# Optimization experiments

Measured on AMD Instinct MI355X. Metric: run time of the kernel, lower is better.

## Reference

```python
import jax, jax.numpy as jnp
import numpy as np

NUM_HEADS = 16
D_MODEL = 1024
HEAD_DIM = D_MODEL // NUM_HEADS
SCALE = float(np.sqrt(HEAD_DIM))  # NOTE: original multiplies q by sqrt(head_dim)
EPS = 1e-5


def layernorm(x, g, b):
    # LayerNorm over last dim (head_dim), learnable affine
    mu = jnp.mean(x, axis=-1, keepdims=True)
    var = jnp.mean(jnp.square(x - mu), axis=-1, keepdims=True)
    return (x - mu) * jax.lax.rsqrt(var + EPS) * g + b


def setup_inputs() -> dict:
    key = jax.random.key(0)
    ks = jax.random.split(key, 8)
    B, Nq, Nc = 2, 2048, 2048
    s = 0.02
    return {
        "x_query": jax.random.normal(ks[0], (B, Nq, D_MODEL), jnp.float32),
        "x_context": jax.random.normal(ks[1], (B, Nc, D_MODEL), jnp.float32),
        "Wq": jax.random.normal(ks[2], (D_MODEL, D_MODEL), jnp.float32) * s,
        "Wkv": jax.random.normal(ks[3], (D_MODEL, 2 * D_MODEL), jnp.float32) * s,
        "Wp": jax.random.normal(ks[4], (D_MODEL, D_MODEL), jnp.float32) * s,
        "bp": jnp.zeros((D_MODEL,), jnp.float32),
        "ln_g": jnp.ones((HEAD_DIM,), jnp.float32),
        "ln_b": jnp.zeros((HEAD_DIM,), jnp.float32),
    }


def reference(x_query, x_context, Wq, Wkv, Wp, bp, ln_g, ln_b):
    B, Nq, _ = x_query.shape
    Nc = x_context.shape[1]
    H, D = NUM_HEADS, HEAD_DIM
    # projections
    q = (x_query @ Wq).reshape(B, Nq, H, D).transpose(0, 2, 1, 3)  # b h n d
    kv = (x_context @ Wkv).reshape(B, Nc, 2, H, D)
    k = kv[:, :, 0].transpose(0, 2, 1, 3)  # b h n d
    v = kv[:, :, 1].transpose(0, 2, 1, 3)
    # QK-LayerNorm (shared params)
    q = layernorm(q, ln_g, ln_b)
    k = layernorm(k, ln_g, ln_b)
    # NOTE: faithful to source — q is MULTIPLIED by sqrt(head_dim)
    q = q * SCALE
    attn = jnp.einsum("bhqd,bhkd->bhqk", q, k)
    attn = jax.nn.softmax(attn, axis=-1)
    out = jnp.einsum("bhqk,bhkd->bhqd", attn, v)
    out = out.transpose(0, 2, 1, 3).reshape(B, Nq, H * D)
    return out @ Wp + bp
```

## Files before the change

### kernel.cpp

```cpp
#include <hip/hip_runtime.h>
#include <stdint.h>

#define NUM_HEADS 16
#define HEAD_DIM 64
#define D_MODEL 1024
#define SEQ 2048
#define BATCH 2

typedef unsigned short u16;
typedef _Float16 f16x8 __attribute__((ext_vector_type(8)));
typedef float f32x4 __attribute__((ext_vector_type(4)));

__device__ __forceinline__ u16 f2h(float f) {
    _Float16 h = (_Float16)f;
    return __builtin_bit_cast(u16, h);
}
__device__ __forceinline__ float h2f(u16 h) {
    return (float)__builtin_bit_cast(_Float16, h);
}
__device__ __forceinline__ uint32_t pkrtz(float a, float b) {
    return __builtin_bit_cast(uint32_t, __builtin_amdgcn_cvt_pkrtz(a, b));
}
__device__ __forceinline__ uint32_t pkrtn(float a, float b) {
    return (uint32_t)f2h(a) | ((uint32_t)f2h(b) << 16);
}

__device__ __forceinline__ float ex2(float x) {
#if __has_builtin(__builtin_amdgcn_exp2f)
    return __builtin_amdgcn_exp2f(x);
#else
    float r;
    asm("v_exp_f32 %0, %1" : "=v"(r) : "v"(x));
    return r;
#endif
}

__device__ __forceinline__ f16x8 ld8h(const u16* p) {
    return *reinterpret_cast<const f16x8*>(p);
}

__device__ __forceinline__ void gl_lds16(const void* g, void* l) {
    __builtin_amdgcn_global_load_lds(
        (const __attribute__((address_space(1))) void*)g,
        (__attribute__((address_space(3))) void*)l,
        16, 0, 0);
}

template <int CTRL>
__device__ __forceinline__ float dpp_mov(float x) {
    return __builtin_bit_cast(float,
        __builtin_amdgcn_update_dpp(0, __builtin_bit_cast(int, x), CTRL, 0xf, 0xf, true));
}
__device__ __forceinline__ float rowsum16(float x) {
    x += dpp_mov<0x121>(x);
    x += dpp_mov<0x122>(x);
    x += dpp_mov<0x124>(x);
    x += dpp_mov<0x128>(x);
    return x;
}

__global__ __launch_bounds__(256) void k_prep(const float* __restrict__ xq,
                                              const float* __restrict__ xc,
                                              const float* __restrict__ Wq,
                                              const float* __restrict__ Wkv,
                                              const float* __restrict__ Wp,
                                              u16* __restrict__ xq16,
                                              u16* __restrict__ xc16,
                                              u16* __restrict__ WqT16,
                                              u16* __restrict__ WkvT16,
                                              u16* __restrict__ WpT16) {
    __shared__ float tile[32][33];
    const int t = blockIdx.x;
    if (t < 8192) {
        int i = t * 256 + threadIdx.x;
        const float* src; u16* dst; int j;
        if (i < 1048576) { src = xq; dst = xq16; j = i; }
        else             { src = xc; dst = xc16; j = i - 1048576; }
        float4 v = reinterpret_cast<const float4*>(src)[j];
        ushort4 o;
        o.x = f2h(v.x); o.y = f2h(v.y); o.z = f2h(v.z); o.w = f2h(v.w);
        reinterpret_cast<ushort4*>(dst)[j] = o;
        return;
    }
    const float* W; u16* WT; int N, bi;
    if (t < 9216)       { W = Wq;  WT = WqT16;  N = 1024; bi = t - 8192; }
    else if (t < 11264) { W = Wkv; WT = WkvT16; N = 2048; bi = t - 9216; }
    else                { W = Wp;  WT = WpT16;  N = 1024; bi = t - 11264; }
    const int K = 1024;
    const int nb = N / 32;
    const int bn = (bi % nb) * 32, bk = (bi / nb) * 32;
    const int tx = threadIdx.x & 31;
    const int ty = threadIdx.x >> 5;
#pragma unroll
    for (int i = 0; i < 32; i += 8)
        tile[ty + i][tx] = W[(size_t)(bk + ty + i) * N + bn + tx];
    __syncthreads();
#pragma unroll
    for (int i = 0; i < 32; i += 8)
        WT[(size_t)(bn + ty + i) * K + bk + tx] = f2h(tile[tx][ty + i]);
}

__device__ __forceinline__ void gemm_mainloop_f16(const u16* __restrict__ A,
                                                  const u16* __restrict__ Bt,
                                                  u16* As, u16* Bs,
                                                  int tileM, int tileN, int K,
                                                  f32x4 acc[4][4]) {
    const int tid = threadIdx.x;
    const int lane = tid & 63;
    const int wv = tid >> 6;
    const int wm = wv >> 1, wn = wv & 1;
    const int quad = lane >> 4, l15 = lane & 15;

    const int c0 = tid, c1 = tid + 256;
    const u16* Ap0 = A + (size_t)(tileM + (c0 >> 2)) * K + (c0 & 3) * 8;
    const u16* Ap1 = A + (size_t)(tileM + (c1 >> 2)) * K + (c1 & 3) * 8;
    const u16* Bp0 = Bt + (size_t)(tileN + (c0 >> 2)) * K + (c0 & 3) * 8;
    const u16* Bp1 = Bt + (size_t)(tileN + (c1 >> 2)) * K + (c1 & 3) * 8;

    gl_lds16(Ap0, &As[c0 * 8]);
    gl_lds16(Ap1, &As[c1 * 8]);
    gl_lds16(Bp0, &Bs[c0 * 8]);
    gl_lds16(Bp1, &Bs[c1 * 8]);

    for (int k0 = 0; k0 < K; k0 += 32) {
        __syncthreads();
        const int cb = (k0 >> 5) & 1;
        if (k0 + 32 < K) {
            const int nbuf = cb ^ 1;
            gl_lds16(Ap0 + k0 + 32, &As[nbuf * 4096 + c0 * 8]);
            gl_lds16(Ap1 + k0 + 32, &As[nbuf * 4096 + c1 * 8]);
            gl_lds16(Bp0 + k0 + 32, &Bs[nbuf * 4096 + c0 * 8]);
            gl_lds16(Bp1 + k0 + 32, &Bs[nbuf * 4096 + c1 * 8]);
        }
        const int cbo = cb * 4096;
        f16x8 af[4], bfr[4];
#pragma unroll
        for (int mi = 0; mi < 4; ++mi)
            af[mi] = ld8h(&As[cbo + (wm * 64 + mi * 16 + l15) * 32 + quad * 8]);
#pragma unroll
        for (int ni = 0; ni < 4; ++ni)
            bfr[ni] = ld8h(&Bs[cbo + (wn * 64 + ni * 16 + l15) * 32 + quad * 8]);
#pragma unroll
        for (int mi = 0; mi < 4; ++mi)
#pragma unroll
            for (int ni = 0; ni < 4; ++ni)
                acc[mi][ni] = __builtin_amdgcn_mfma_f32_16x16x32_f16(
                    af[mi], bfr[ni], acc[mi][ni], 0, 0, 0);
    }
}

#define ACC_INIT()                                                   \
    f32x4 acc[4][4];                                                 \
    _Pragma("unroll") for (int i = 0; i < 4; ++i)                    \
        _Pragma("unroll") for (int j = 0; j < 4; ++j)                \
            acc[i][j] = (f32x4){0.f, 0.f, 0.f, 0.f};

__global__ __launch_bounds__(256, 2) void k_proj_f16(const u16* __restrict__ xq16,
                                                     const u16* __restrict__ xc16,
                                                     const u16* __restrict__ WqT16,
                                                     const u16* __restrict__ WkvT16,
                                                     const float* __restrict__ lng,
                                                     const float* __restrict__ lnb,
                                                     u16* __restrict__ Qh_h,
                                                     u16* __restrict__ Qh_l,
                                                     u16* __restrict__ Kh,
                                                     u16* __restrict__ VT) {
    __shared__ __align__(16) u16 As[2 * 128 * 32];
    __shared__ __align__(16) u16 Bs[2 * 128 * 32];
    const int bx = blockIdx.x;
    const int tileM = blockIdx.y * 128;
    const int tid = threadIdx.x;
    const int lane = tid & 63;
    const int wv = tid >> 6;
    const int wm = wv >> 1, wn = wv & 1;
    const int quad = lane >> 4, l15 = lane & 15;
    ACC_INIT();

    if (bx < 16) {
        const bool isQ = bx < 8;
        const int tileN = (bx & 7) * 128;
        const u16* Axx = isQ ? xq16 : xc16;
        const u16* Bt  = isQ ? WqT16 : WkvT16;
        const float scl = isQ ? 11.5415603294809528f : 1.0f;

        gemm_mainloop_f16(Axx, Bt, As, Bs, tileM, tileN, D_MODEL, acc);

        float gv[4], bv[4];
#pragma unroll
        for (int ni = 0; ni < 4; ++ni) { gv[ni] = lng[ni * 16 + l15]; bv[ni] = lnb[ni * 16 + l15]; }

#pragma unroll
        for (int mi = 0; mi < 4; ++mi) {
#pragma unroll
            for (int r = 0; r < 4; ++r) {
                float sum = 0.f, sq = 0.f;
#pragma unroll
                for (int ni = 0; ni < 4; ++ni) { float x = acc[mi][ni][r]; sum += x; sq += x * x; }
                sum = rowsum16(sum);
                sq  = rowsum16(sq);
                float mu = sum * (1.f / 64.f);
                float var = sq * (1.f / 64.f) - mu * mu;
                float rs = rsqrtf(var + 1e-5f);
                int m = tileM + wm * 64 + mi * 16 + quad * 4 + r;
                int bb = m >> 11, n = m & (SEQ - 1);
#pragma unroll
                for (int ni = 0; ni < 4; ++ni) {
                    int colg = tileN + wn * 64 + ni * 16 + l15;
                    int h = colg >> 6;
                    float y = ((acc[mi][ni][r] - mu) * rs * gv[ni] + bv[ni]) * scl;
                    size_t idx = (((size_t)bb * NUM_HEADS + h) * SEQ + n) * HEAD_DIM + (colg & 63);
                    u16 yh = f2h(y);
                    if (isQ) {
                        Qh_h[idx] = yh;
                        Qh_l[idx] = f2h(y - h2f(yh));
                    } else {
                        Kh[idx] = yh;
                    }
                }
            }
        }
    } else {
        const int tileN = D_MODEL + (bx - 16) * 128;
        gemm_mainloop_f16(xc16, WkvT16, As, Bs, tileM, tileN, D_MODEL, acc);
#pragma unroll
        for (int mi = 0; mi < 4; ++mi) {
            int m0 = tileM + wm * 64 + mi * 16 + quad * 4;
            int bb = m0 >> 11, n0 = m0 & (SEQ - 1);
#pragma unroll
            for (int ni = 0; ni < 4; ++ni) {
                int colg = tileN + wn * 64 + ni * 16 + l15 - D_MODEL;
                int h = colg >> 6, d = colg & 63;
                ushort4 o;
                o.x = f2h(acc[mi][ni][0]);
                o.y = f2h(acc[mi][ni][1]);
                o.z = f2h(acc[mi][ni][2]);
                o.w = f2h(acc[mi][ni][3]);
                *reinterpret_cast<ushort4*>(
                    &VT[(((size_t)bb * NUM_HEADS + h) * HEAD_DIM + d) * SEQ + n0]) = o;
            }
        }
    }
}

__global__ __launch_bounds__(256, 2) void k_gemm_out(const u16* __restrict__ A,
                                                     const u16* __restrict__ Bt,
                                                     const float* __restrict__ bp,
                                                     float* __restrict__ out) {
    __shared__ __align__(16) u16 As[2 * 128 * 32];
    __shared__ __align__(16) u16 Bs[2 * 128 * 32];
    const int tileM = blockIdx.y * 128, tileN = blockIdx.x * 128;
    const int tid = threadIdx.x;
    const int lane = tid & 63;
    const int wv = tid >> 6;
    const int wm = wv >> 1, wn = wv & 1;
    const int quad = lane >> 4, l15 = lane & 15;
    ACC_INIT();
    gemm_mainloop_f16(A, Bt, As, Bs, tileM, tileN, D_MODEL, acc);

    float bpv[4];
#pragma unroll
    for (int ni = 0; ni < 4; ++ni) bpv[ni] = bp[tileN + wn * 64 + ni * 16 + l15];
#pragma unroll
    for (int mi = 0; mi < 4; ++mi) {
#pragma unroll
        for (int r = 0; r < 4; ++r) {
            int m = tileM + wm * 64 + mi * 16 + quad * 4 + r;
#pragma unroll
            for (int ni = 0; ni < 4; ++ni) {
                int colg = tileN + wn * 64 + ni * 16 + l15;
                out[(size_t)m * D_MODEL + colg] = acc[mi][ni][r] + bpv[ni];
            }
        }
    }
}

__global__ __launch_bounds__(256) void k_attn(const u16* __restrict__ Qh_h,
                                              const u16* __restrict__ Qh_l,
                                              const u16* __restrict__ Kh,
                                              const u16* __restrict__ VT,
                                              u16* __restrict__ AO) {
    __shared__ __align__(16) u16 Ks[2 * 64 * 64];
    __shared__ __align__(16) u16 Vs[2 * 64 * 64];
    __shared__ __align__(16) u16 Ps[64 * 64];

    const int tid = threadIdx.x;
    const int lane = tid & 63;
    const int wv = tid >> 6;
    const int quad = lane >> 4, l15 = lane & 15;
    const int sw = l15 & 3;
    const int w1 = (l15 >> 2) & 1;
    const int id = blockIdx.x;
    const int bh = (id & 7) | (((id >> 8) & 3) << 3);
    const int qt = (id >> 3) & 31;

    const size_t bh_off = (size_t)bh * SEQ * HEAD_DIM;
    const u16* Vbh = VT + (size_t)bh * HEAD_DIM * SEQ;

    f16x8 qfh[2], qfl[2];
#pragma unroll
    for (int kt = 0; kt < 2; ++kt) {
        size_t off = bh_off + (size_t)(qt * 64 + wv * 16 + l15) * HEAD_DIM + kt * 32 + quad * 8;
        qfh[kt] = ld8h(Qh_h + off);
        qfl[kt] = ld8h(Qh_l + off);
    }

    f16x8 ones;
#pragma unroll
    for (int i = 0; i < 8; ++i) ones[i] = (_Float16)1.0f;

    const int rr = lane >> 3;
    const int ss = lane & 7;
    const int cc = ss ^ rr;
    const int row0 = wv * 16 + rr;
    const u16* k0 = Kh + bh_off + (size_t)row0 * HEAD_DIM + cc * 8;
    const u16* v0 = Vbh + (size_t)row0 * SEQ + cc * 8;
    const int ldsW = (wv * 16) * 64;

    f32x4 acc_o[4];
    f32x4 acc_l = (f32x4){0.f, 0.f, 0.f, 0.f};
    float m_i = -3.0e38f;
#pragma unroll
    for (int ni = 0; ni < 4; ++ni) acc_o[ni] = (f32x4){0.f, 0.f, 0.f, 0.f};

    gl_lds16(k0,                &Ks[ldsW]);
    gl_lds16(k0 + 8 * HEAD_DIM, &Ks[ldsW + 8 * 64]);
    gl_lds16(v0,                &Vs[ldsW]);
    gl_lds16(v0 + 8 * SEQ,      &Vs[ldsW + 8 * 64]);

    const int psRow = (wv * 16 + l15) * 64;
    const int psW = psRow + (quad ^ (w1 << 1)) * 4;

    for (int j = 0; j < SEQ / 64; ++j) {
        __syncthreads();
        if (j + 1 < SEQ / 64) {
            const int nb = (j + 1) & 1;
            const size_t ko = (size_t)(j + 1) * 64 * HEAD_DIM;
            const int vo = (j + 1) * 64;
            gl_lds16(k0 + ko,                &Ks[nb * 4096 + ldsW]);
            gl_lds16(k0 + ko + 8 * HEAD_DIM, &Ks[nb * 4096 + ldsW + 8 * 64]);
            gl_lds16(v0 + vo,                &Vs[nb * 4096 + ldsW]);
            gl_lds16(v0 + vo + 8 * SEQ,      &Vs[nb * 4096 + ldsW + 8 * 64]);
        }
        const int bb = (j & 1) * 4096;

        f32x4 acc_s[4];
#pragma unroll
        for (int ni = 0; ni < 4; ++ni) acc_s[ni] = (f32x4){0.f, 0.f, 0.f, 0.f};
#pragma unroll
        for (int kt = 0; kt < 2; ++kt) {
            f16x8 kf[4];
#pragma unroll
            for (int ni = 0; ni < 4; ++ni) {
                int slot = (kt * 4 + quad) ^ (l15 & 7);
                kf[ni] = ld8h(&Ks[bb + (ni * 16 + l15) * 64 + slot * 8]);
            }
#pragma unroll
            for (int ni = 0; ni < 4; ++ni) {
                acc_s[ni] = __builtin_amdgcn_mfma_f32_16x16x32_f16(
                    kf[ni], qfh[kt], acc_s[ni], 0, 0, 0);
                acc_s[ni] = __builtin_amdgcn_mfma_f32_16x16x32_f16(
                    kf[ni], qfl[kt], acc_s[ni], 0, 0, 0);
            }
        }

        float mn[4];
#pragma unroll
        for (int ni = 0; ni < 4; ++ni)
            mn[ni] = fmaxf(fmaxf(acc_s[ni][0], acc_s[ni][1]),
                           fmaxf(acc_s[ni][2], acc_s[ni][3]));
        float mx = fmaxf(fmaxf(mn[0], mn[1]), fmaxf(mn[2], mn[3]));
        mx = fmaxf(mx, __shfl_xor(mx, 16, 64));
        mx = fmaxf(mx, __shfl_xor(mx, 32, 64));
        float mnew = fmaxf(m_i, mx);
        if (__any(mx > m_i)) {
            float alpha = ex2(m_i - mnew);
#pragma unroll
            for (int ni = 0; ni < 4; ++ni) acc_o[ni] *= alpha;
            acc_l[0] *= alpha;
            m_i = mnew;
        }
#pragma unroll
        for (int ni = 0; ni < 4; ++ni) {
            float p0 = ex2(acc_s[ni][0] - mnew);
            float p1 = ex2(acc_s[ni][1] - mnew);
            float p2 = ex2(acc_s[ni][2] - mnew);
            float p3 = ex2(acc_s[ni][3] - mnew);
            uint2 u;
            u.x = pkrtz(p0, p1);
            u.y = pkrtz(p2, p3);
            *reinterpret_cast<uint2*>(&Ps[psW + ((ni ^ sw) * 16)]) = u;
        }

#pragma unroll
        for (int kt = 0; kt < 2; ++kt) {
            int pchunk = (kt * 2 + (quad >> 1)) ^ sw;
            f16x8 pf = ld8h(&Ps[psRow + pchunk * 16 + (((quad & 1) ^ w1) * 8)]);
            f16x8 vf[4];
#pragma unroll
            for (int ni = 0; ni < 4; ++ni) {
                int slot = (kt * 4 + quad) ^ (l15 & 7);
                vf[ni] = ld8h(&Vs[bb + (ni * 16 + l15) * 64 + slot * 8]);
            }
#pragma unroll
            for (int ni = 0; ni < 4; ++ni)
                acc_o[ni] = __builtin_amdgcn_mfma_f32_16x16x32_f16(
                    vf[ni], pf, acc_o[ni], 0, 0, 0);
            acc_l = __builtin_amdgcn_mfma_f32_16x16x32_f16(
                ones, pf, acc_l, 0, 0, 0);
        }
    }

    const float inv = 1.0f / acc_l[0];
#pragma unroll
    for (int ni = 0; ni < 4; ++ni) {
        uint2 u;
        u.x = pkrtn(acc_o[ni][0] * inv, acc_o[ni][1] * inv);
        u.y = pkrtn(acc_o[ni][2] * inv, acc_o[ni][3] * inv);
        *reinterpret_cast<uint2*>(&Ps[psW + ((ni ^ sw) * 16)]) = u;
    }
    const int b = bh >> 4, h = bh & 15;
    const int qrow = qt * 64 + wv * 16 + l15;
    const int echunk = quad ^ sw;
    uint4 o0 = *reinterpret_cast<const uint4*>(&Ps[psRow + echunk * 16 + w1 * 8]);
    uint4 o1 = *reinterpret_cast<const uint4*>(&Ps[psRow + echunk * 16 + (1 - w1) * 8]);
    size_t outb = ((size_t)(b * SEQ + qrow)) * D_MODEL + h * 64 + quad * 16;
    *reinterpret_cast<uint4*>(&AO[outb])     = o0;
    *reinterpret_cast<uint4*>(&AO[outb + 8]) = o1;
}

extern "C" void kernel_launch(void* const* d_in, const int* in_sizes, int n_in,
                              void* d_out, int out_size, void* d_ws, size_t ws_size,
                              hipStream_t stream) {
    const float* xq  = (const float*)d_in[0];
    const float* xc  = (const float*)d_in[1];
    const float* Wq  = (const float*)d_in[2];
    const float* Wkv = (const float*)d_in[3];
    const float* Wp  = (const float*)d_in[4];
    const float* bp  = (const float*)d_in[5];
    const float* lng = (const float*)d_in[6];
    const float* lnb = (const float*)d_in[7];
    float* out = (float*)d_out;

    char* ws = (char*)d_ws;
    const size_t MB = 1 << 20;
    u16* xq16   = (u16*)(ws + 0 * MB);
    u16* xc16   = (u16*)(ws + 8 * MB);
    u16* WqT16  = (u16*)(ws + 16 * MB);
    u16* WkvT16 = (u16*)(ws + 18 * MB);
    u16* WpT16  = (u16*)(ws + 22 * MB);
    u16* Qh_h   = (u16*)(ws + 24 * MB);
    u16* Qh_l   = (u16*)(ws + 32 * MB);
    u16* Kh     = (u16*)(ws + 40 * MB);
    u16* VT     = (u16*)(ws + 48 * MB);
    u16* AO     = xq16;

    k_prep<<<12288, 256, 0, stream>>>(xq, xc, Wq, Wkv, Wp,
                                      xq16, xc16, WqT16, WkvT16, WpT16);
    k_proj_f16<<<dim3(24, 32), 256, 0, stream>>>(xq16, xc16, WqT16, WkvT16,
                                                 lng, lnb, Qh_h, Qh_l, Kh, VT);
    k_attn<<<1024, 256, 0, stream>>>(Qh_h, Qh_l, Kh, VT, AO);
    k_gemm_out<<<dim3(8, 32), 256, 0, stream>>>(AO, WpT16, bp, out);
}
```

Before: 241.4 us.

## Remap GEMM blocks per XCD, shrink output GEMM tile, raise attention MFMA priority

The projection and output GEMMs now use a flat 1D grid that maps consecutive M tiles onto the same XCD, so blocks sharing rows of A hit the same L2. The output GEMM moves to 128x64 tiles with its own mainloop, doubling the block count to 512 so the GPU's compute units fill better. The attention kernel wraps its two MFMA phases in s_setprio(1) to favour matrix issue over other waves. The smaller output tile lowers per-block reuse, and the priority hints may or may not help scheduling.

```diff
diff --git a/kernel.cpp b/kernel.cpp
--- a/kernel.cpp
+++ b/kernel.cpp
@@ -167,8 +167,11 @@
                                                      u16* __restrict__ VT) {
     __shared__ __align__(16) u16 As[2 * 128 * 32];
     __shared__ __align__(16) u16 Bs[2 * 128 * 32];
-    const int bx = blockIdx.x;
-    const int tileM = blockIdx.y * 128;
+    const int flat = blockIdx.x;
+    const int xcd = flat & 7;
+    const int j = flat >> 3;
+    const int bx = j >> 2;
+    const int tileM = (xcd * 4 + (j & 3)) * 128;
     const int tid = threadIdx.x;
     const int lane = tid & 63;
     const int wv = tid >> 6;
@@ -247,27 +250,70 @@
                                                      const float* __restrict__ bp,
                                                      float* __restrict__ out) {
     __shared__ __align__(16) u16 As[2 * 128 * 32];
-    __shared__ __align__(16) u16 Bs[2 * 128 * 32];
-    const int tileM = blockIdx.y * 128, tileN = blockIdx.x * 128;
+    __shared__ __align__(16) u16 Bs[2 * 64 * 32];
+    const int flat = blockIdx.x;
+    const int xcd = flat & 7;
+    const int j = flat >> 3;
+    const int tileM = (xcd * 4 + (j & 3)) * 128;
+    const int tileN = (j >> 2) * 64;
     const int tid = threadIdx.x;
     const int lane = tid & 63;
     const int wv = tid >> 6;
     const int wm = wv >> 1, wn = wv & 1;
     const int quad = lane >> 4, l15 = lane & 15;
-    ACC_INIT();
-    gemm_mainloop_f16(A, Bt, As, Bs, tileM, tileN, D_MODEL, acc);
-
-    float bpv[4];
-#pragma unroll
-    for (int ni = 0; ni < 4; ++ni) bpv[ni] = bp[tileN + wn * 64 + ni * 16 + l15];
+    const int K = D_MODEL;
+
+    f32x4 acc[4][2];
+#pragma unroll
+    for (int i = 0; i < 4; ++i)
+#pragma unroll
+        for (int n = 0; n < 2; ++n) acc[i][n] = (f32x4){0.f, 0.f, 0.f, 0.f};
+
+    const int c0 = tid, c1 = tid + 256;
+    const u16* Ap0 = A + (size_t)(tileM + (c0 >> 2)) * K + (c0 & 3) * 8;
+    const u16* Ap1 = A + (size_t)(tileM + (c1 >> 2)) * K + (c1 & 3) * 8;
+    const u16* Bp0 = Bt + (size_t)(tileN + (c0 >> 2)) * K + (c0 & 3) * 8;
+
+    gl_lds16(Ap0, &As[c0 * 8]);
+    gl_lds16(Ap1, &As[c1 * 8]);
+    gl_lds16(Bp0, &Bs[c0 * 8]);
+
+    for (int k0 = 0; k0 < K; k0 += 32) {
+        __syncthreads();
+        const int cb = (k0 >> 5) & 1;
+        if (k0 + 32 < K) {
+            const int nbuf = cb ^ 1;
+            gl_lds16(Ap0 + k0 + 32, &As[nbuf * 4096 + c0 * 8]);
+            gl_lds16(Ap1 + k0 + 32, &As[nbuf * 4096 + c1 * 8]);
+            gl_lds16(Bp0 + k0 + 32, &Bs[nbuf * 2048 + c0 * 8]);
+        }
+        const int ao = cb * 4096, bo = cb * 2048;
+        f16x8 af[4], bfr[2];
+#pragma unroll
+        for (int mi = 0; mi < 4; ++mi)
+            af[mi] = ld8h(&As[ao + (wm * 64 + mi * 16 + l15) * 32 + quad * 8]);
+#pragma unroll
+        for (int ni = 0; ni < 2; ++ni)
+            bfr[ni] = ld8h(&Bs[bo + (wn * 32 + ni * 16 + l15) * 32 + quad * 8]);
+#pragma unroll
+        for (int mi = 0; mi < 4; ++mi)
+#pragma unroll
+            for (int ni = 0; ni < 2; ++ni)
+                acc[mi][ni] = __builtin_amdgcn_mfma_f32_16x16x32_f16(
+                    af[mi], bfr[ni], acc[mi][ni], 0, 0, 0);
+    }
+
+    float bpv[2];
+#pragma unroll
+    for (int ni = 0; ni < 2; ++ni) bpv[ni] = bp[tileN + wn * 32 + ni * 16 + l15];
 #pragma unroll
     for (int mi = 0; mi < 4; ++mi) {
 #pragma unroll
         for (int r = 0; r < 4; ++r) {
             int m = tileM + wm * 64 + mi * 16 + quad * 4 + r;
 #pragma unroll
-            for (int ni = 0; ni < 4; ++ni) {
-                int colg = tileN + wn * 64 + ni * 16 + l15;
+            for (int ni = 0; ni < 2; ++ni) {
+                int colg = tileN + wn * 32 + ni * 16 + l15;
                 out[(size_t)m * D_MODEL + colg] = acc[mi][ni][r] + bpv[ni];
             }
         }
@@ -346,6 +392,7 @@
         f32x4 acc_s[4];
 #pragma unroll
         for (int ni = 0; ni < 4; ++ni) acc_s[ni] = (f32x4){0.f, 0.f, 0.f, 0.f};
+        __builtin_amdgcn_s_setprio(1);
 #pragma unroll
         for (int kt = 0; kt < 2; ++kt) {
             f16x8 kf[4];
@@ -362,6 +409,7 @@
                     kf[ni], qfl[kt], acc_s[ni], 0, 0, 0);
             }
         }
+        __builtin_amdgcn_s_setprio(0);
 
         float mn[4];
 #pragma unroll
@@ -391,6 +439,7 @@
             *reinterpret_cast<uint2*>(&Ps[psW + ((ni ^ sw) * 16)]) = u;
         }
 
+        __builtin_amdgcn_s_setprio(1);
 #pragma unroll
         for (int kt = 0; kt < 2; ++kt) {
             int pchunk = (kt * 2 + (quad >> 1)) ^ sw;
@@ -408,6 +457,7 @@
             acc_l = __builtin_amdgcn_mfma_f32_16x16x32_f16(
                 ones, pf, acc_l, 0, 0, 0);
         }
+        __builtin_amdgcn_s_setprio(0);
     }
 
     const float inv = 1.0f / acc_l[0];
@@ -456,8 +506,8 @@
 
     k_prep<<<12288, 256, 0, stream>>>(xq, xc, Wq, Wkv, Wp,
                                       xq16, xc16, WqT16, WkvT16, WpT16);
-    k_proj_f16<<<dim3(24, 32), 256, 0, stream>>>(xq16, xc16, WqT16, WkvT16,
-                                                 lng, lnb, Qh_h, Qh_l, Kh, VT);
+    k_proj_f16<<<768, 256, 0, stream>>>(xq16, xc16, WqT16, WkvT16,
+                                        lng, lnb, Qh_h, Qh_l, Kh, VT);
     k_attn<<<1024, 256, 0, stream>>>(Qh_h, Qh_l, Kh, VT, AO);
-    k_gemm_out<<<dim3(8, 32), 256, 0, stream>>>(AO, WpT16, bp, out);
-}
+    k_gemm_out<<<512, 256, 0, stream>>>(AO, WpT16, bp, out);
+}
```

Result: slower. 250.2 us (+3.7%).
